# Performance work log

Measured on AMD Instinct MI355X. Metric: run time of the kernel, lower is better.

The kernel has to match this reference:

```python
import jax, jax.numpy as jnp
import numpy as np

M, K, N = 8192, 1024, 8192

def setup_inputs() -> dict:
    key = jax.random.key(0)
    k1, k2, k3, k4 = jax.random.split(key, 4)
    # a, b are int8-valued quantized tensors (stored as int32 per harness dtype set)
    a = jax.random.randint(k1, (M, K), 0, 127, dtype=jnp.int32)
    b = jax.random.randint(k2, (K, N), 0, 127, dtype=jnp.int32)
    alpha_row = jax.random.uniform(k3, (M, 1), dtype=jnp.float32)
    alpha_col = jax.random.uniform(k4, (1, N), dtype=jnp.float32)
    return {"a": a, "b": b, "alpha_row": alpha_row, "alpha_col": alpha_col}

def reference(a, b, alpha_row, alpha_col):
    # Faithful to TorchGemmA8W8.forward: upcast int8 operands to fp32,
    # matmul with fp32 accumulate, cast result to int8.
    # (alpha_row / alpha_col are accepted but unused in this variant.)
    x = jnp.matmul(a.astype(jnp.float32), b.astype(jnp.float32))  # [M, N] fp32
    return x.astype(jnp.int8)
```

## Files before the change

kernel.cpp:

```cpp
#include <hip/hip_runtime.h>
#include <stdint.h>

#define M_DIM 8192
#define N_DIM 8192
#define K_DIM 1024
#define BK    128

typedef int int4v __attribute__((ext_vector_type(4)));

__device__ __forceinline__ void gload16(const char* g, char* l) {
    __builtin_amdgcn_global_load_lds(
        (__attribute__((address_space(1))) void*)(void*)const_cast<char*>(g),
        (__attribute__((address_space(3))) void*)l,
        16, 0, 0);
}

__device__ __forceinline__ int sat8(int v) {
    v = v > 127 ? 127 : v;
    v = v < -128 ? -128 : v;
    return v;
}

__global__ __launch_bounds__(256) void pack_ab_kernel(const int* __restrict__ a,
                                                      const int* __restrict__ b,
                                                      int* __restrict__ outA,
                                                      char* __restrict__ outB) {
    __shared__ char tile[64][68];
    const int t = threadIdx.x;
    if (blockIdx.x < 8192) {
        int i = blockIdx.x * 256 + t;
        int4 v = ((const int4*)a)[i];
        outA[i] = (v.x & 0xff) | ((v.y & 0xff) << 8) |
                  ((v.z & 0xff) << 16) | ((v.w & 0xff) << 24);
        return;
    }
    const int bx = blockIdx.x - 8192;
    const int n0 = (bx & 127) * 64;
    const int k0 = (bx >> 7) * 64;
    const int tr  = t >> 4;
    const int tc4 = (t & 15) << 2;
#pragma unroll
    for (int j = 0; j < 4; ++j) {
        int row = tr + j * 16;
        int4 v = *(const int4*)&b[(size_t)(k0 + row) * N_DIM + n0 + tc4];
        tile[row][tc4 + 0] = (char)v.x;
        tile[row][tc4 + 1] = (char)v.y;
        tile[row][tc4 + 2] = (char)v.z;
        tile[row][tc4 + 3] = (char)v.w;
    }
    __syncthreads();
#pragma unroll
    for (int j = 0; j < 4; ++j) {
        int n = tr + j * 16;
        int pk = (tile[tc4 + 0][n] & 0xff) |
                 ((tile[tc4 + 1][n] & 0xff) << 8) |
                 ((tile[tc4 + 2][n] & 0xff) << 16) |
                 ((tile[tc4 + 3][n] & 0xff) << 24);
        *(int*)&outB[(size_t)(n0 + n) * K_DIM + k0 + tc4] = pk;
    }
}

__global__ __launch_bounds__(256) void gemm_i8_kernel(const char* __restrict__ A8,
                                                      const char* __restrict__ B8,
                                                      int* __restrict__ C) {
    __shared__ __align__(16) char As[2 * 128 * 64];
    __shared__ __align__(16) char Bs[2 * 128 * 64];

    const int t    = threadIdx.x;
    const int bn   = blockIdx.x;
    const int bm   = blockIdx.y;
    const int lane = t & 63;
    const int wave = t >> 6;
    const int wm   = wave >> 1;
    const int wn   = wave & 1;
    const int quad = lane >> 4;
    const int l16  = lane & 15;

    const size_t aBase = (size_t)(bm * 128) * K_DIM;
    const size_t bBase = (size_t)(bn * 128) * K_DIM;

    const int sr = t >> 2;
    const int sc = (t & 3) << 4;

    int4v acc[4][4] = {};

    for (int kt = 0; kt < K_DIM / BK; ++kt) {
        const int kOff = kt * BK;
#pragma unroll
        for (int s = 0; s < 4; ++s) {
            const int p = s >> 1;
            const int rr = ((s & 1) << 6) + sr;
            const int f = s * 4096 + t * 16;
            gload16(A8 + aBase + (size_t)rr * K_DIM + kOff + p * 64 + sc, As + f);
            gload16(B8 + bBase + (size_t)rr * K_DIM + kOff + p * 64 + sc, Bs + f);
        }
        __syncthreads();

#pragma unroll
        for (int h = 0; h < 2; ++h) {
            int4v af[4], bf[4];
#pragma unroll
            for (int mi = 0; mi < 4; ++mi)
                af[mi] = *(const int4v*)
                    &As[h * 8192 + (wm * 64 + mi * 16 + l16) * 64 + quad * 16];
#pragma unroll
            for (int ni = 0; ni < 4; ++ni)
                bf[ni] = *(const int4v*)
                    &Bs[h * 8192 + (wn * 64 + ni * 16 + l16) * 64 + quad * 16];

#pragma unroll
            for (int mi = 0; mi < 4; ++mi)
#pragma unroll
                for (int ni = 0; ni < 4; ++ni)
                    acc[mi][ni] = __builtin_amdgcn_mfma_i32_16x16x64_i8(
                        af[mi], bf[ni], acc[mi][ni], 0, 0, 0);
        }

        __syncthreads();
    }

    const int mBase = bm * 128 + wm * 64;
    const int nBase = bn * 128 + wn * 64;
#pragma unroll
    for (int mi = 0; mi < 4; ++mi) {
#pragma unroll
        for (int ni = 0; ni < 4; ++ni) {
            const int col = nBase + ni * 16 + l16;
#pragma unroll
            for (int r = 0; r < 4; ++r) {
                const int row = mBase + mi * 16 + quad * 4 + r;
                C[(size_t)row * N_DIM + col] = sat8(acc[mi][ni][r]);
            }
        }
    }
}

__global__ __launch_bounds__(256) void gemm_naive_kernel(const int* __restrict__ a,
                                                         const int* __restrict__ b,
                                                         int* __restrict__ C) {
    const int col = blockIdx.x * 256 + threadIdx.x;
    const int row = blockIdx.y;
    int acc = 0;
    for (int k = 0; k < K_DIM; ++k)
        acc += a[(size_t)row * K_DIM + k] * b[(size_t)k * N_DIM + col];
    C[(size_t)row * N_DIM + col] = sat8(acc);
}

extern "C" void kernel_launch(void* const* d_in, const int* in_sizes, int n_in,
                              void* d_out, int out_size, void* d_ws, size_t ws_size,
                              hipStream_t stream) {
    const int* a = (const int*)d_in[0];
    const int* b = (const int*)d_in[1];
    int* out = (int*)d_out;

    const size_t needed = 2 * (size_t)M_DIM * K_DIM;
    if (ws_size < needed) {
        gemm_naive_kernel<<<dim3(N_DIM / 256, M_DIM), 256, 0, stream>>>(a, b, out);
        return;
    }

    char* A8 = (char*)d_ws;
    char* B8 = A8 + (size_t)M_DIM * K_DIM;

    pack_ab_kernel<<<8192 + 2048, 256, 0, stream>>>(a, b, (int*)A8, B8);
    gemm_i8_kernel<<<dim3(N_DIM / 128, M_DIM / 128), 256, 0, stream>>>(A8, B8, out);
}
```

Baseline: 364.8 us.

## Rewrite int8 GEMM with 256x256 tiles, swizzled LDS and pipelined phases

```diff
diff --git a/kernel.cpp b/kernel.cpp
--- a/kernel.cpp
+++ b/kernel.cpp
@@ -60,69 +60,97 @@
     }
 }
 
-__global__ __launch_bounds__(256) void gemm_i8_kernel(const char* __restrict__ A8,
-                                                      const char* __restrict__ B8,
-                                                      int* __restrict__ C) {
-    __shared__ __align__(16) char As[2 * 128 * 64];
-    __shared__ __align__(16) char Bs[2 * 128 * 64];
+__device__ __forceinline__ void stage_half(const char* __restrict__ gbase,
+                                           char* lds, int t, int ktile, int kk) {
+#pragma unroll
+    for (int i = 0; i < 2; ++i) {
+        const int s   = t + i * 512;
+        const int row = s >> 2;
+        const int cc  = (s & 3) ^ ((row >> 1) & 3);
+        gload16(gbase + ((size_t)row << 10) + ((size_t)(ktile & 7) << 7)
+                      + (kk << 6) + (cc << 4),
+                lds + s * 16);
+    }
+}
+
+#define PHASE(BUF, KK, MIH, LOADB, VMW, STG) do {                                   \
+    int4v af0 = *(const int4v*)&As[BUF][KK][aRow + ((MIH)*4+0)*16][laneByte];       \
+    int4v af1 = *(const int4v*)&As[BUF][KK][aRow + ((MIH)*4+1)*16][laneByte];       \
+    int4v af2 = *(const int4v*)&As[BUF][KK][aRow + ((MIH)*4+2)*16][laneByte];       \
+    int4v af3 = *(const int4v*)&As[BUF][KK][aRow + ((MIH)*4+3)*16][laneByte];       \
+    if (LOADB) {                                                                    \
+        bf[0] = *(const int4v*)&Bs[BUF][KK][bRow + 0*16][laneByte];                 \
+        bf[1] = *(const int4v*)&Bs[BUF][KK][bRow + 1*16][laneByte];                 \
+        bf[2] = *(const int4v*)&Bs[BUF][KK][bRow + 2*16][laneByte];                 \
+        bf[3] = *(const int4v*)&Bs[BUF][KK][bRow + 3*16][laneByte];                 \
+    }                                                                               \
+    STG;                                                                            \
+    __builtin_amdgcn_s_barrier();                                                   \
+    asm volatile("s_waitcnt lgkmcnt(0)" ::: "memory");                              \
+    __builtin_amdgcn_sched_barrier(0);       \
+    __builtin_amdgcn_s_setprio(1);                                                  \
+    _Pragma("unroll")                                                               \
+    for (int ni = 0; ni < 4; ++ni) {                                                \
+        acc[(MIH)*4+0][ni] = __builtin_amdgcn_mfma_i32_16x16x64_i8(af0, bf[ni], acc[(MIH)*4+0][ni], 0,0,0); \
+        acc[(MIH)*4+1][ni] = __builtin_amdgcn_mfma_i32_16x16x64_i8(af1, bf[ni], acc[(MIH)*4+1][ni], 0,0,0); \
+        acc[(MIH)*4+2][ni] = __builtin_amdgcn_mfma_i32_16x16x64_i8(af2, bf[ni], acc[(MIH)*4+2][ni], 0,0,0); \
+        acc[(MIH)*4+3][ni] = __builtin_amdgcn_mfma_i32_16x16x64_i8(af3, bf[ni], acc[(MIH)*4+3][ni], 0,0,0); \
+    }                                                                               \
+    __builtin_amdgcn_s_setprio(0);                                                  \
+    if (VMW) asm volatile("s_waitcnt vmcnt(8)" ::: "memory");                       \
+    __builtin_amdgcn_s_barrier();                                                   \
+} while (0)
+
+__global__ __launch_bounds__(512, 2) void gemm_i8_kernel(const char* __restrict__ A8,
+                                                         const char* __restrict__ B8,
+                                                         int* __restrict__ C) {
+    __shared__ __align__(16) char As[2][2][256][64];
+    __shared__ __align__(16) char Bs[2][2][256][64];
 
     const int t    = threadIdx.x;
     const int bn   = blockIdx.x;
     const int bm   = blockIdx.y;
     const int lane = t & 63;
     const int wave = t >> 6;
-    const int wm   = wave >> 1;
-    const int wn   = wave & 1;
+    const int wm   = wave >> 2;
+    const int wn   = wave & 3;
     const int quad = lane >> 4;
     const int l16  = lane & 15;
+    const int laneByte = ((quad ^ ((l16 >> 1) & 3)) << 4);
+    const int aRow = wm * 128 + l16;
+    const int bRow = wn * 64 + l16;
 
-    const size_t aBase = (size_t)(bm * 128) * K_DIM;
-    const size_t bBase = (size_t)(bn * 128) * K_DIM;
+    const char* aG = A8 + (size_t)(bm * 256) * K_DIM;
+    const char* bG = B8 + (size_t)(bn * 256) * K_DIM;
 
-    const int sr = t >> 2;
-    const int sc = (t & 3) << 4;
+    int4v acc[8][4] = {};
+    int4v bf[4];
 
-    int4v acc[4][4] = {};
+    stage_half(aG, &As[0][0][0][0], t, 0, 0);
+    stage_half(bG, &Bs[0][0][0][0], t, 0, 0);
+    stage_half(aG, &As[0][1][0][0], t, 0, 1);
+    stage_half(bG, &Bs[0][1][0][0], t, 0, 1);
+    stage_half(aG, &As[1][0][0][0], t, 1, 0);
+    stage_half(bG, &Bs[1][0][0][0], t, 1, 0);
+    asm volatile("s_waitcnt vmcnt(8)" ::: "memory");
+    __builtin_amdgcn_s_barrier();
 
-    for (int kt = 0; kt < K_DIM / BK; ++kt) {
-        const int kOff = kt * BK;
-#pragma unroll
-        for (int s = 0; s < 4; ++s) {
-            const int p = s >> 1;
-            const int rr = ((s & 1) << 6) + sr;
-            const int f = s * 4096 + t * 16;
-            gload16(A8 + aBase + (size_t)rr * K_DIM + kOff + p * 64 + sc, As + f);
-            gload16(B8 + bBase + (size_t)rr * K_DIM + kOff + p * 64 + sc, Bs + f);
-        }
-        __syncthreads();
-
-#pragma unroll
-        for (int h = 0; h < 2; ++h) {
-            int4v af[4], bf[4];
-#pragma unroll
-            for (int mi = 0; mi < 4; ++mi)
-                af[mi] = *(const int4v*)
-                    &As[h * 8192 + (wm * 64 + mi * 16 + l16) * 64 + quad * 16];
-#pragma unroll
-            for (int ni = 0; ni < 4; ++ni)
-                bf[ni] = *(const int4v*)
-                    &Bs[h * 8192 + (wn * 64 + ni * 16 + l16) * 64 + quad * 16];
-
-#pragma unroll
-            for (int mi = 0; mi < 4; ++mi)
-#pragma unroll
-                for (int ni = 0; ni < 4; ++ni)
-                    acc[mi][ni] = __builtin_amdgcn_mfma_i32_16x16x64_i8(
-                        af[mi], bf[ni], acc[mi][ni], 0, 0, 0);
-        }
-
-        __syncthreads();
+#pragma unroll 1
+    for (int j = 0; j < K_DIM / BK / 2; ++j) {
+        PHASE(0,0,0, 1, 0, stage_half(aG, &As[1][1][0][0], t, 2*j+1, 1));
+        PHASE(0,0,1, 0, 1, stage_half(bG, &Bs[1][1][0][0], t, 2*j+1, 1));
+        PHASE(0,1,0, 1, 0, stage_half(aG, &As[0][0][0][0], t, 2*j+2, 0));
+        PHASE(0,1,1, 0, 1, stage_half(bG, &Bs[0][0][0][0], t, 2*j+2, 0));
+        PHASE(1,0,0, 1, 0, stage_half(aG, &As[0][1][0][0], t, 2*j+2, 1));
+        PHASE(1,0,1, 0, 1, stage_half(bG, &Bs[0][1][0][0], t, 2*j+2, 1));
+        PHASE(1,1,0, 1, 0, stage_half(aG, &As[1][0][0][0], t, 2*j+3, 0));
+        PHASE(1,1,1, 0, 1, stage_half(bG, &Bs[1][0][0][0], t, 2*j+3, 0));
     }
 
-    const int mBase = bm * 128 + wm * 64;
-    const int nBase = bn * 128 + wn * 64;
+    const int mBase = bm * 256 + wm * 128;
+    const int nBase = bn * 256 + wn * 64;
 #pragma unroll
-    for (int mi = 0; mi < 4; ++mi) {
+    for (int mi = 0; mi < 8; ++mi) {
 #pragma unroll
         for (int ni = 0; ni < 4; ++ni) {
             const int col = nBase + ni * 16 + l16;
@@ -163,5 +191,5 @@
     char* B8 = A8 + (size_t)M_DIM * K_DIM;
 
     pack_ab_kernel<<<8192 + 2048, 256, 0, stream>>>(a, b, (int*)A8, B8);
-    gemm_i8_kernel<<<dim3(N_DIM / 128, M_DIM / 128), 256, 0, stream>>>(A8, B8, out);
+    gemm_i8_kernel<<<dim3(N_DIM / 256, M_DIM / 256), 512, 0, stream>>>(A8, B8, out);
 }
```

New measurement: 397.6 us. 1.09x slower.
